# Performance work log

Measured on AMD Instinct MI355X. Metric: run time of the kernel, lower is better.

## Reference

```python
import jax, jax.numpy as jnp
import numpy as np

COMMITMENT_COST = 0.25

def setup_inputs() -> dict:
    key = jax.random.key(0)
    k1, k2 = jax.random.split(key)
    B, C, H, W = 16, 256, 32, 32
    K = 8192
    z = jax.random.normal(k1, (B, C, H, W), dtype=jnp.float32)
    # torch init: uniform(-1/codebook_size, 1/codebook_size)
    embedding = jax.random.uniform(k2, (K, C), dtype=jnp.float32,
                                   minval=-1.0 / K, maxval=1.0 / K)
    return {"z": z, "embedding": embedding}


def reference(z, embedding):
    # z: [B, C, H, W] -> [B, H, W, C]
    z = jnp.transpose(z, (0, 2, 3, 1))
    B, H, W, C = z.shape
    zf = z.reshape(-1, C)  # [N, C]

    # squared euclidean distances: [N, K]
    d = (jnp.sum(zf * zf, axis=1, keepdims=True)
         + jnp.sum(embedding * embedding, axis=1)
         - 2.0 * jnp.einsum('nc,kc->nk', zf, embedding))
    idx = jnp.argmin(d, axis=1)  # [N]

    z_q = embedding[idx].reshape(B, H, W, C)

    commitment_loss = COMMITMENT_COST * (jax.lax.stop_gradient(z_q) - z) ** 2
    codebook_loss = (z_q - jax.lax.stop_gradient(z)) ** 2
    loss = commitment_loss + codebook_loss  # [B, H, W, C]

    # straight-through estimator
    z_q = z + jax.lax.stop_gradient(z_q - z)
    z_q = jnp.transpose(z_q, (0, 3, 1, 2))  # back to [B, C, H, W]
    return z_q, loss, idx
```

## Files before the change

### kernel.cpp

```cpp
#include <hip/hip_runtime.h>
#include <hip/hip_bf16.h>


#define NROWS 16384
#define KCODES 8192

__global__ void k_zz(const float* __restrict__ z, float* __restrict__ zz){
  __shared__ float p[256];
  const int t  = threadIdx.x;
  const int nl = t & 63, q = t >> 6;
  const int n  = blockIdx.x * 64 + nl;
  const int b  = n >> 10, hw = n & 1023;
  const float* zp = z + b * 262144 + hw;
  float s = 0.f;
  const int c0 = q * 64;
  #pragma unroll 8
  for (int i = 0; i < 64; ++i){
    float v = zp[(c0 + i) * 1024];
    s = fmaf(v, v, s);
  }
  p[t] = s;
  __syncthreads();
  if (q == 0){
    float tot = ((p[nl] + p[nl + 64]) + p[nl + 128]) + p[nl + 192];
    zz[n] = tot;
  }
}

__global__ void k_ee(const float* __restrict__ emb, float* __restrict__ ee){
  const int t = threadIdx.x;
  const int k = blockIdx.x * 4 + (t >> 6);
  const int lane = t & 63;
  const float* ep = emb + k * 256;
  float s = 0.f;
  #pragma unroll
  for (int j = 0; j < 4; ++j){
    float v = ep[lane + 64 * j];
    s = fmaf(v, v, s);
  }
  #pragma unroll
  for (int off = 32; off; off >>= 1) s += __shfl_down(s, off);
  if (lane == 0) ee[k] = s;
}

__global__ __launch_bounds__(256, 1)
void k_argmin(const float* __restrict__ z, const float* __restrict__ emb,
              const float* __restrict__ zz, const float* __restrict__ ee,
              float* __restrict__ candd, int* __restrict__ candi){
  __shared__ float zs[128][36];
  __shared__ float es[128][36];

  const int tid = threadIdx.x;
  const int bid = blockIdx.x;
  const int rowblock = bid >> 2;
  const int quarter  = bid & 3;
  const int n0     = rowblock * 128;
  const int k0base = quarter * 2048;
  const int tx = tid & 15, ty = tid >> 4;

  const int b = n0 >> 10, hw0 = n0 & 1023;
  const float* zb = z + b * 262144 + hw0;

  float acc[8][8];
  float best[8];
  int   bidx[8];
  float zzr[8];
  #pragma unroll
  for (int i = 0; i < 8; ++i){
    best[i] = 3.0e38f; bidx[i] = 0;
    zzr[i]  = zz[n0 + ty * 8 + i];
    #pragma unroll
    for (int j = 0; j < 8; ++j) acc[i][j] = 0.f;
  }

  for (int kt = 0; kt < 16; ++kt){
    const int kk0 = k0base + kt * 128;
    for (int cc = 0; cc < 8; ++cc){
      const int cbase = cc * 32;
      float4 zr[4], er[4];
      #pragma unroll
      for (int l = 0; l < 4; ++l){
        const int idx = tid + 256 * l;
        const int c = idx >> 5, ng = idx & 31;
        zr[l] = *reinterpret_cast<const float4*>(zb + (cbase + c) * 1024 + ng * 4);
      }
      #pragma unroll
      for (int l = 0; l < 4; ++l){
        const int idx = tid + 256 * l;
        const int k = idx >> 3, cg = idx & 7;
        er[l] = *reinterpret_cast<const float4*>(emb + (kk0 + k) * 256 + cbase + cg * 4);
      }
      __syncthreads();
      #pragma unroll
      for (int l = 0; l < 4; ++l){
        const int idx = tid + 256 * l;
        const int c = idx >> 5, ng = idx & 31;
        const float v[4] = {zr[l].x, zr[l].y, zr[l].z, zr[l].w};
        #pragma unroll
        for (int m = 0; m < 4; ++m){
          const int r = ng * 4 + m;
          const int g = ((r >> 2) & 7) ^ ((r >> 5) & 3);
          zs[r][4 * ((c >> 2) ^ g) + (c & 3)] = v[m];
        }
      }
      #pragma unroll
      for (int l = 0; l < 4; ++l){
        const int idx = tid + 256 * l;
        const int k = idx >> 3, cg = idx & 7;
        const int cgs = cg ^ ((k >> 3) & 7);
        *reinterpret_cast<float4*>(&es[k][cgs * 4]) = er[l];
      }
      __syncthreads();
      #pragma unroll
      for (int s4 = 0; s4 < 8; ++s4){
        float4 ev[8];
        #pragma unroll
        for (int j = 0; j < 8; ++j){
          const int k = tx * 8 + j;
          ev[j] = *reinterpret_cast<const float4*>(&es[k][4 * (s4 ^ (tx & 7))]);
        }
        #pragma unroll
        for (int i = 0; i < 8; ++i){
          const int r = ty * 8 + i;
          const int g = ((r >> 2) & 7) ^ ((r >> 5) & 3);
          const float4 zv = *reinterpret_cast<const float4*>(&zs[r][4 * (s4 ^ g)]);
          #pragma unroll
          for (int j = 0; j < 8; ++j){
            float a = acc[i][j];
            a = fmaf(zv.x, ev[j].x, a);
            a = fmaf(zv.y, ev[j].y, a);
            a = fmaf(zv.z, ev[j].z, a);
            a = fmaf(zv.w, ev[j].w, a);
            acc[i][j] = a;
          }
        }
      }
    }
    float eeg[8];
    #pragma unroll
    for (int j = 0; j < 8; ++j) eeg[j] = ee[kk0 + tx * 8 + j];
    #pragma unroll
    for (int i = 0; i < 8; ++i){
      #pragma unroll
      for (int j = 0; j < 8; ++j){
        const float t1 = zzr[i] + eeg[j];
        const float d  = t1 - 2.0f * acc[i][j];
        const int kidx = kk0 + tx * 8 + j;
        if (d < best[i]) { best[i] = d; bidx[i] = kidx; }
        acc[i][j] = 0.f;
      }
    }
  }

  __syncthreads();
  float* redd = &zs[0][0];
  int*   redi = reinterpret_cast<int*>(&es[0][0]);
  #pragma unroll
  for (int i = 0; i < 8; ++i){
    const int r = ty * 8 + i;
    redd[r * 16 + tx] = best[i];
    redi[r * 16 + tx] = bidx[i];
  }
  __syncthreads();
  if (tid < 128){
    const int r = tid;
    float bd = redd[r * 16];
    int   bi = redi[r * 16];
    #pragma unroll
    for (int t2 = 1; t2 < 16; ++t2){
      const float d = redd[r * 16 + t2];
      const int  ii = redi[r * 16 + t2];
      if (d < bd || (d == bd && ii < bi)) { bd = d; bi = ii; }
    }
    candd[(n0 + r) * 4 + quarter] = bd;
    candi[(n0 + r) * 4 + quarter] = bi;
  }
}

__global__ void k_pick(const float* __restrict__ candd, const int* __restrict__ candi,
                       int* __restrict__ idx32, float* __restrict__ out_idx){
  const int n = blockIdx.x * 256 + threadIdx.x;
  float bd = candd[n * 4];
  int   bi = candi[n * 4];
  #pragma unroll
  for (int t = 1; t < 4; ++t){
    const float d = candd[n * 4 + t];
    const int  ii = candi[n * 4 + t];
    if (d < bd) { bd = d; bi = ii; }
  }
  bi &= (KCODES - 1);
  idx32[n] = bi;
  out_idx[n] = (float)bi;
}

__global__ void k_zq(const float* __restrict__ z, const float* __restrict__ emb,
                     const int* __restrict__ idx32, float* __restrict__ out_zq){
  const int bid = blockIdx.x;
  const int b = bid >> 8, c = bid & 255;
  const int t = threadIdx.x;
  const float* zp = z + b * 262144 + c * 1024;
  #pragma unroll
  for (int l = 0; l < 4; ++l){
    const int hw = t + 256 * l;
    const float zv = zp[hw];
    const int  ii  = idx32[b * 1024 + hw] & (KCODES - 1);
    const float e  = emb[ii * 256 + c];
    const float s  = e - zv;
    out_zq[b * 262144 + c * 1024 + hw] = zv + s;
  }
}

__global__ void k_loss(const float* __restrict__ z, const float* __restrict__ emb,
                       const int* __restrict__ idx32, float* __restrict__ out_loss){
  __shared__ float zt[256][33];
  __shared__ int   li[32];
  const int bid = blockIdx.x;
  const int b = bid >> 5, h = bid & 31;
  const int t = threadIdx.x;
  const float* zp = z + b * 262144 + h * 32;
  #pragma unroll 4
  for (int l = 0; l < 32; ++l){
    const int idx = t + 256 * l;
    const int c = idx >> 5, w = idx & 31;
    zt[c][w] = zp[c * 1024 + w];
  }
  if (t < 32) li[t] = idx32[b * 1024 + h * 32 + t] & (KCODES - 1);
  __syncthreads();
  const int c = t;
  const long obase = (long)((b * 32 + h) * 32) * 256;
  for (int w = 0; w < 32; ++w){
    const float zv = zt[c][w];
    const float e  = emb[li[w] * 256 + c];
    const float s  = e - zv;
    const float t2 = s * s;
    out_loss[obase + (long)w * 256 + c] = 0.25f * t2 + t2;
  }
}

extern "C" void kernel_launch(void* const* d_in, const int* in_sizes, int n_in,
                              void* d_out, int out_size, void* d_ws, size_t ws_size,
                              hipStream_t stream) {
  const float* z   = (const float*)d_in[0];
  const float* emb = (const float*)d_in[1];

  float* out      = (float*)d_out;
  float* out_zq   = out;
  float* out_loss = out + 4194304;
  float* out_idx  = out + 8388608;

  float* zzp   = (float*)d_ws;
  float* eep   = zzp + NROWS;
  int*   idx32 = (int*)(eep + KCODES);
  float* candd = (float*)(idx32 + NROWS);
  int*   candi = (int*)(candd + NROWS * 4);

  k_zz    <<<256, 256, 0, stream>>>(z, zzp);
  k_ee    <<<2048, 256, 0, stream>>>(emb, eep);
  k_argmin<<<512, 256, 0, stream>>>(z, emb, zzp, eep, candd, candi);
  k_pick  <<<64, 256, 0, stream>>>(candd, candi, idx32, out_idx);
  k_zq    <<<4096, 256, 0, stream>>>(z, emb, idx32, out_zq);
  k_loss  <<<512, 256, 0, stream>>>(z, emb, idx32, out_loss);
}
```

Baseline: 1.185 ms.

## Double-buffer LDS tiles in argmin GEMM and prefetch next chunk during compute

```diff
diff --git a/kernel.cpp b/kernel.cpp
--- a/kernel.cpp
+++ b/kernel.cpp
@@ -43,12 +43,13 @@
   if (lane == 0) ee[k] = s;
 }
 
-__global__ __launch_bounds__(256, 1)
+__global__ __launch_bounds__(256)
+__attribute__((amdgpu_waves_per_eu(1, 2)))
 void k_argmin(const float* __restrict__ z, const float* __restrict__ emb,
               const float* __restrict__ zz, const float* __restrict__ ee,
               float* __restrict__ candd, int* __restrict__ candi){
-  __shared__ float zs[128][36];
-  __shared__ float es[128][36];
+  __shared__ float zs[2][128][36];
+  __shared__ float es[2][128][40];
 
   const int tid = threadIdx.x;
   const int bid = blockIdx.x;
@@ -73,88 +74,107 @@
     for (int j = 0; j < 8; ++j) acc[i][j] = 0.f;
   }
 
-  for (int kt = 0; kt < 16; ++kt){
+  float4 zr[4], er[4];
+
+  auto gload = [&](int chunk){
+    const int kt = chunk >> 3, cc = chunk & 7;
+    const int cbase = cc * 32;
     const int kk0 = k0base + kt * 128;
-    for (int cc = 0; cc < 8; ++cc){
-      const int cbase = cc * 32;
-      float4 zr[4], er[4];
-      #pragma unroll
-      for (int l = 0; l < 4; ++l){
-        const int idx = tid + 256 * l;
-        const int c = idx >> 5, ng = idx & 31;
-        zr[l] = *reinterpret_cast<const float4*>(zb + (cbase + c) * 1024 + ng * 4);
-      }
-      #pragma unroll
-      for (int l = 0; l < 4; ++l){
-        const int idx = tid + 256 * l;
-        const int k = idx >> 3, cg = idx & 7;
-        er[l] = *reinterpret_cast<const float4*>(emb + (kk0 + k) * 256 + cbase + cg * 4);
-      }
-      __syncthreads();
-      #pragma unroll
-      for (int l = 0; l < 4; ++l){
-        const int idx = tid + 256 * l;
-        const int c = idx >> 5, ng = idx & 31;
-        const float v[4] = {zr[l].x, zr[l].y, zr[l].z, zr[l].w};
-        #pragma unroll
-        for (int m = 0; m < 4; ++m){
-          const int r = ng * 4 + m;
-          const int g = ((r >> 2) & 7) ^ ((r >> 5) & 3);
-          zs[r][4 * ((c >> 2) ^ g) + (c & 3)] = v[m];
-        }
-      }
-      #pragma unroll
-      for (int l = 0; l < 4; ++l){
-        const int idx = tid + 256 * l;
-        const int k = idx >> 3, cg = idx & 7;
-        const int cgs = cg ^ ((k >> 3) & 7);
-        *reinterpret_cast<float4*>(&es[k][cgs * 4]) = er[l];
-      }
-      __syncthreads();
-      #pragma unroll
-      for (int s4 = 0; s4 < 8; ++s4){
-        float4 ev[8];
+    #pragma unroll
+    for (int l = 0; l < 4; ++l){
+      const int idx = tid + 256 * l;
+      const int c = idx >> 5, ng = idx & 31;
+      zr[l] = *reinterpret_cast<const float4*>(zb + (cbase + c) * 1024 + ng * 4);
+    }
+    #pragma unroll
+    for (int l = 0; l < 4; ++l){
+      const int idx = tid + 256 * l;
+      const int k = idx >> 3, cg = idx & 7;
+      er[l] = *reinterpret_cast<const float4*>(emb + (kk0 + k) * 256 + cbase + cg * 4);
+    }
+  };
+
+  auto dswrite = [&](int buf){
+    #pragma unroll
+    for (int l = 0; l < 4; ++l){
+      const int idx = tid + 256 * l;
+      const int c = idx >> 5, ng = idx & 31;
+      const float v[4] = {zr[l].x, zr[l].y, zr[l].z, zr[l].w};
+      #pragma unroll
+      for (int m = 0; m < 4; ++m){
+        const int r = ng * 4 + m;
+        const int g = ((r >> 2) & 7) ^ ((r >> 5) & 3);
+        zs[buf][r][4 * ((c >> 2) ^ g) + (c & 3)] = v[m];
+      }
+    }
+    #pragma unroll
+    for (int l = 0; l < 4; ++l){
+      const int idx = tid + 256 * l;
+      const int k = idx >> 3, cg = idx & 7;
+      const int cgs = cg ^ ((k >> 3) & 7);
+      *reinterpret_cast<float4*>(&es[buf][k][cgs * 4]) = er[l];
+    }
+  };
+
+  gload(0);
+  dswrite(0);
+  __syncthreads();
+
+  for (int chunk = 0; chunk < 128; ++chunk){
+    const int buf = chunk & 1;
+    if (chunk < 127) gload(chunk + 1);
+
+    #pragma unroll
+    for (int s4 = 0; s4 < 8; ++s4){
+      float4 ev[8];
+      #pragma unroll
+      for (int j = 0; j < 8; ++j){
+        const int k = tx * 8 + j;
+        ev[j] = *reinterpret_cast<const float4*>(&es[buf][k][4 * (s4 ^ (tx & 7))]);
+      }
+      #pragma unroll
+      for (int i = 0; i < 8; ++i){
+        const int r = ty * 8 + i;
+        const int g = ((r >> 2) & 7) ^ ((r >> 5) & 3);
+        const float4 zv = *reinterpret_cast<const float4*>(&zs[buf][r][4 * (s4 ^ g)]);
         #pragma unroll
         for (int j = 0; j < 8; ++j){
-          const int k = tx * 8 + j;
-          ev[j] = *reinterpret_cast<const float4*>(&es[k][4 * (s4 ^ (tx & 7))]);
+          float a = acc[i][j];
+          a = fmaf(zv.x, ev[j].x, a);
+          a = fmaf(zv.y, ev[j].y, a);
+          a = fmaf(zv.z, ev[j].z, a);
+          a = fmaf(zv.w, ev[j].w, a);
+          acc[i][j] = a;
         }
+      }
+    }
+
+    if ((chunk & 7) == 7){
+      const int kt  = chunk >> 3;
+      const int kk0 = k0base + kt * 128;
+      float eeg[8];
+      #pragma unroll
+      for (int j = 0; j < 8; ++j) eeg[j] = ee[kk0 + tx * 8 + j];
+      #pragma unroll
+      for (int i = 0; i < 8; ++i){
         #pragma unroll
-        for (int i = 0; i < 8; ++i){
-          const int r = ty * 8 + i;
-          const int g = ((r >> 2) & 7) ^ ((r >> 5) & 3);
-          const float4 zv = *reinterpret_cast<const float4*>(&zs[r][4 * (s4 ^ g)]);
-          #pragma unroll
-          for (int j = 0; j < 8; ++j){
-            float a = acc[i][j];
-            a = fmaf(zv.x, ev[j].x, a);
-            a = fmaf(zv.y, ev[j].y, a);
-            a = fmaf(zv.z, ev[j].z, a);
-            a = fmaf(zv.w, ev[j].w, a);
-            acc[i][j] = a;
-          }
+        for (int j = 0; j < 8; ++j){
+          const float t1 = zzr[i] + eeg[j];
+          const float d  = t1 - 2.0f * acc[i][j];
+          const int kidx = kk0 + tx * 8 + j;
+          if (d < best[i]) { best[i] = d; bidx[i] = kidx; }
+          acc[i][j] = 0.f;
         }
       }
     }
-    float eeg[8];
-    #pragma unroll
-    for (int j = 0; j < 8; ++j) eeg[j] = ee[kk0 + tx * 8 + j];
-    #pragma unroll
-    for (int i = 0; i < 8; ++i){
-      #pragma unroll
-      for (int j = 0; j < 8; ++j){
-        const float t1 = zzr[i] + eeg[j];
-        const float d  = t1 - 2.0f * acc[i][j];
-        const int kidx = kk0 + tx * 8 + j;
-        if (d < best[i]) { best[i] = d; bidx[i] = kidx; }
-        acc[i][j] = 0.f;
-      }
-    }
-  }
-
-  __syncthreads();
-  float* redd = &zs[0][0];
-  int*   redi = reinterpret_cast<int*>(&es[0][0]);
+
+    __syncthreads();
+    if (chunk < 127) dswrite(buf ^ 1);
+    __syncthreads();
+  }
+
+  float* redd = &zs[0][0][0];
+  int*   redi = reinterpret_cast<int*>(&es[0][0][0]);
   #pragma unroll
   for (int i = 0; i < 8; ++i){
     const int r = ty * 8 + i;
```

New measurement: 1.263 ms. 1.07x slower.
